# Optimization experiments

Measured on AMD Instinct MI355X. Metric: run time of the kernel, lower is better.

## Reference

```python
import jax, jax.numpy as jnp
import numpy as np
from jax import lax

NF = 64; LAT = 512; IMG = 64; NC = 4
DILS = (1, 2, 4, 8)                 # dilated 3x3 sobel: effective kernels 3,5,9,17 w/ pads 1,2,4,8
CF = 1 + 2 * len(DILS)              # identity + (sobel_x, sobel_y) per scale -> 9
FIN = NF * CF; FH = NF; FO = NF     # DynaResidualBlock dims
NFREQ = 6; FCH = 4 * NFREQ          # sin/cos over x and y per frequency -> 24 pos channels
CAT = LAT + NF * FCH                # input dim of out_to_lat blocks (512 + 1536 = 2048)
P_DYN = FH * FIN + FH + FO * FH + FO + FO * FIN + FO


def _make_pe():
    c = (np.arange(IMG, dtype=np.float32) + 0.5) / IMG
    yy, xx = np.meshgrid(c, c, indexing='ij')
    ch = []
    for u in (xx, yy):
        for f in range(NFREQ):
            w = (2.0 ** f) * 2.0 * np.pi
            ch.append(np.sin(w * u)); ch.append(np.cos(w * u))
    return jnp.asarray(np.stack(ch, 0).astype(np.float32))   # [FCH, H, W]


def _lin_res(x, w1, b1, w2, b2, ws, bs):
    # LinearResidualBlock: skip linear + 2-layer MLP with LeakyReLU(0.2)
    return x @ ws + bs + jax.nn.leaky_relu(x @ w1 + b1, 0.2) @ w2 + b2

_SX = jnp.array([[-1., 0., 1.], [-2., 0., 2.], [-1., 0., 1.]], jnp.float32) / 8.0
_SY = _SX.T


def _perceive(x):
    # multi-scale sobel perception (RandGrads): identity + depthwise dilated sobel x/y
    feats = [x]
    dn = ('NCHW', 'OIHW', 'NCHW')
    for d in DILS:
        for k in (_SX, _SY):
            kern = jnp.broadcast_to(k, (NF, 1, 3, 3))
            feats.append(lax.conv_general_dilated(
                x, kern, (1, 1), [(d, d), (d, d)],
                rhs_dilation=(d, d), dimension_numbers=dn,
                feature_group_count=NF))
    return jnp.concatenate(feats, axis=1)   # [B, NF*CF, H, W]


def _inorm(x, eps=1e-5):
    # InstanceNorm2d (affine=False)
    m = x.mean((2, 3), keepdims=True)
    v = ((x - m) ** 2).mean((2, 3), keepdims=True)
    return (x - m) * lax.rsqrt(v + eps)


def _dyna_conv(x, lat, dyn_w, dyn_b):
    # DynaResidualBlock: hypernetwork generates per-sample 1x1 conv weights from lat
    B = x.shape[0]
    p = lat @ dyn_w + dyn_b                 # [B, P_DYN]
    o = 0
    def take(n):
        nonlocal o
        q = p[:, o:o + n]; o += n; return q
    k_in = take(FH * FIN).reshape(B, FH, FIN); b_in = take(FH)
    k_out = take(FO * FH).reshape(B, FO, FH); b_out = take(FO)
    k_sk = take(FO * FIN).reshape(B, FO, FIN); b_sk = take(FO)
    h = jnp.einsum('bfi,bihw->bfhw', k_in, x) + b_in[:, :, None, None]
    h = jax.nn.leaky_relu(h, 0.2)
    y = jnp.einsum('bof,bfhw->bohw', k_out, h) + b_out[:, :, None, None]
    s = jnp.einsum('boi,bihw->bohw', k_sk, x) + b_sk[:, :, None, None]
    return s + y


def setup_inputs() -> dict:
    key = jax.random.key(0)
    ks = jax.random.split(key, 16)
    g = lambda i, shape, s=0.02: jax.random.normal(ks[i], shape, jnp.float32) * s
    z = lambda shape: jnp.zeros(shape, jnp.float32)
    return {
        'x': jax.random.normal(ks[0], (16, 3, IMG, IMG), jnp.float32),
        'inj_lat': jax.random.normal(ks[1], (16, LAT), jnp.float32),
        'w_in': g(2, (NF, 3), 0.3), 'b_in': z((NF,)),
        'fl_w1': g(3, (LAT, LAT)), 'fl_b1': z((LAT,)),
        'fl_w2': g(4, (LAT, LAT)), 'fl_b2': z((LAT,)),
        'fl_ws': g(5, (LAT, LAT)), 'fl_bs': z((LAT,)),
        'dyn_w': g(6, (LAT, P_DYN), 0.002), 'dyn_b': g(7, (P_DYN,), 0.002),
        'pe': _make_pe(),
        'otl_w1': g(8, (NC, CAT, CAT)), 'otl_b1': z((NC, CAT)),
        'otl_w2': g(9, (NC, CAT, LAT)), 'otl_b2': z((NC, LAT)),
        'otl_ws': g(10, (NC, CAT, LAT)), 'otl_bs': z((NC, LAT)),
        'ltl_w': g(11, (LAT, LAT)), 'ltl_b': z((LAT,)),
    }


def reference(x, inj_lat, w_in, b_in, fl_w1, fl_b1, fl_w2, fl_b2, fl_ws, fl_bs,
              dyn_w, dyn_b, pe, otl_w1, otl_b1, otl_w2, otl_b2, otl_ws, otl_bs,
              ltl_w, ltl_b):
    B = x.shape[0]
    out = jnp.einsum('oc,bchw->bohw', w_in, x) + b_in[None, :, None, None]  # in_conv (1x1)
    lat = jnp.zeros((B, LAT), x.dtype)
    for c in range(NC):
        inj_lat = _lin_res(inj_lat, fl_w1, fl_b1, fl_w2, fl_b2, fl_ws, fl_bs)
        out = _dyna_conv(_inorm(_perceive(out)), inj_lat, dyn_w, dyn_b)
        # ConvFreqEncoding(out).mean((2,3)) == contraction of out with pos encodings
        freq = jnp.einsum('bchw,fhw->bcf', out, pe).reshape(B, -1) / (IMG * IMG)
        lat = _lin_res(jnp.concatenate([lat, freq], axis=1),
                       otl_w1[c], otl_b1[c], otl_w2[c], otl_b2[c], otl_ws[c], otl_bs[c])
    return lat @ ltl_w + ltl_b
```

## Files before the change

### kernel.cpp

```cpp
#include <hip/hip_runtime.h>
#include <hip/hip_bf16.h>
#include <cstdint>
#include <cstddef>

#define PIX   4096
#define PDYN  78016
#define LATD  512
#define CATD  2048

typedef unsigned short u16;
typedef __attribute__((ext_vector_type(8))) short bf16x8;
typedef __attribute__((ext_vector_type(4))) float f32x4;
#define MFMA16(a,b,c) __builtin_amdgcn_mfma_f32_16x16x32_bf16(a,b,c,0,0,0)

__device__ __forceinline__ float lrelu(float v) { return v > 0.f ? v : 0.2f * v; }
__device__ __forceinline__ unsigned bfbits(float x) {
  __hip_bfloat16 h = __float2bfloat16(x);
  return (unsigned)*(unsigned short*)&h;
}
__device__ __forceinline__ unsigned pack2(float a, float b) {
  return bfbits(a) | (bfbits(b) << 16);
}

__global__ void k_zero(float* __restrict__ p, int n) {
  int i = blockIdx.x * 256 + threadIdx.x;
  if (i < n) p[i] = 0.f;
}

__global__ void k_init_out(const float* __restrict__ x, const float* __restrict__ w_in,
                           const float* __restrict__ b_in, float* __restrict__ out) {
  int idx = blockIdx.x * 256 + threadIdx.x;
  int p = idx & 4095, o = (idx >> 12) & 63, b = idx >> 18;
  const float* xb = x + (size_t)b * 3 * PIX + p;
  out[idx] = b_in[o] + w_in[o*3+0]*xb[0] + w_in[o*3+1]*xb[PIX] + w_in[o*3+2]*xb[2*PIX];
}

__global__ void k_cat_init(const float* __restrict__ lat, float* __restrict__ cat) {
  int idx = blockIdx.x * 256 + threadIdx.x;
  int j = idx & 2047, b = idx >> 11;
  cat[idx] = (j < 512) ? lat[b*512 + j] : 0.f;
}

__global__ void k_pe(const float* __restrict__ pe, u16* __restrict__ peB) {
  int idx = blockIdx.x * 256 + threadIdx.x;
  int j = idx & 7, lane = (idx >> 3) & 63, kc = (idx >> 9) & 3, ft = (idx >> 11) & 1, pt = idx >> 12;
  int f = ft*16 + (lane & 15);
  int p = pt*128 + kc*32 + (lane >> 4)*8 + j;
  peB[idx] = (f < 24) ? (u16)bfbits(pe[(size_t)f*PIX + p]) : (u16)0;
}

__global__ void k_afold(const float* __restrict__ inj_seq, u16* __restrict__ Abf) {
  int idx = blockIdx.x * 256 + threadIdx.x;
  int j = idx & 7, lane = (idx >> 3) & 63, mt = (idx >> 9) & 3, kc = (idx >> 11) & 1, kb = idx >> 12;
  int m = mt*16 + (lane & 15);
  int k = kb*64 + kc*32 + (lane >> 4)*8 + j;
  Abf[idx] = (u16)bfbits(inj_seq[m*512 + k]);
}

__device__ __forceinline__ void feat9(const float (*ch)[65], int h, int w, float* f) {
  f[0] = ch[h][w];
#pragma unroll
  for (int di = 0; di < 4; ++di) {
    int d = 1 << di;
    bool hm = (h - d) >= 0, hp = (h + d) < 64;
    bool wm = (w - d) >= 0, wp = (w + d) < 64;
    float tm = (hm && wm) ? ch[h-d][w-d] : 0.f;
    float t0 =  hm        ? ch[h-d][w  ] : 0.f;
    float tp = (hm && wp) ? ch[h-d][w+d] : 0.f;
    float mm =  wm        ? ch[h  ][w-d] : 0.f;
    float mp =  wp        ? ch[h  ][w+d] : 0.f;
    float bm = (hp && wm) ? ch[h+d][w-d] : 0.f;
    float b0 =  hp        ? ch[h+d][w  ] : 0.f;
    float bp = (hp && wp) ? ch[h+d][w+d] : 0.f;
    f[1 + 2*di] = (tp - tm + 2.f*(mp - mm) + bp - bm) * 0.125f;
    f[2 + 2*di] = (bm - tm + 2.f*(b0 - t0) + bp - tp) * 0.125f;
  }
}

__global__ __launch_bounds__(256) void k_prep(const float* __restrict__ out,
                                              __hip_bfloat16* __restrict__ xn) {
  __shared__ float ch[64][65];
  __shared__ float redS[4][9], redQ[4][9];
  __shared__ float mS[9], rS[9];
  int c = blockIdx.x, b = blockIdx.y, t = threadIdx.x;
  const float* src = out + ((size_t)b * 64 + c) * PIX;
  for (int j = 0; j < 16; ++j) { int idx = t + j*256; ch[idx >> 6][idx & 63] = src[idx]; }
  __syncthreads();
  float s[9], q[9];
#pragma unroll
  for (int k = 0; k < 9; ++k) { s[k] = 0.f; q[k] = 0.f; }
  for (int j = 0; j < 16; ++j) {
    int p = t + j*256; int h = p >> 6, w = p & 63;
    float f[9]; feat9(ch, h, w, f);
#pragma unroll
    for (int k = 0; k < 9; ++k) { s[k] += f[k]; q[k] += f[k]*f[k]; }
  }
#pragma unroll
  for (int off = 32; off; off >>= 1)
#pragma unroll
    for (int k = 0; k < 9; ++k) { s[k] += __shfl_down(s[k], off, 64); q[k] += __shfl_down(q[k], off, 64); }
  int lane = t & 63, wv = t >> 6;
  if (lane == 0)
#pragma unroll
    for (int k = 0; k < 9; ++k) { redS[wv][k] = s[k]; redQ[wv][k] = q[k]; }
  __syncthreads();
  if (t < 9) {
    float ss = 0.f, qq = 0.f;
    for (int w2 = 0; w2 < 4; ++w2) { ss += redS[w2][t]; qq += redQ[w2][t]; }
    float mean = ss * (1.f/4096.f);
    float var  = qq * (1.f/4096.f) - mean*mean;
    mS[t] = mean; rS[t] = rsqrtf(var + 1e-5f);
  }
  __syncthreads();
  for (int j = 0; j < 16; ++j) {
    int p = t + j*256; int h = p >> 6, w = p & 63;
    float f[9]; feat9(ch, h, w, f);
#pragma unroll
    for (int k = 0; k < 9; ++k)
      xn[((size_t)b * 576 + k*64 + c) * PIX + p] = __float2bfloat16((f[k] - mS[k]) * rS[k]);
  }
}

__global__ __launch_bounds__(256) void k_pgemm(
    const u16* __restrict__ Abf, const float* __restrict__ Bw,
    const float* __restrict__ bias, u16* __restrict__ Wst4,
    u16* __restrict__ KoutF4, float* __restrict__ biasf4) {
  __shared__ u16 Xl[128 * 64];
  int t = threadIdx.x;
  int lane = t & 63, wv = t >> 6;
  int col = lane & 15, quad = lane >> 4;
  int n0 = blockIdx.x * 128;
  int pg = t & 15, kq = t >> 4;

  f32x4 acc[4][2];
#pragma unroll
  for (int i = 0; i < 4; ++i) { acc[i][0] = {0.f,0.f,0.f,0.f}; acc[i][1] = {0.f,0.f,0.f,0.f}; }

  bool vld = (n0 + pg*8) < PDYN;

  for (int kb = 0; kb < 8; ++kb) {
    float br[4][8];
#pragma unroll
    for (int kk = 0; kk < 4; ++kk) {
      const float* src = Bw + (size_t)(kb*64 + kq*4 + kk)*PDYN + n0 + pg*8;
      float4 a0 = vld ? *(const float4*)src       : float4{0.f,0.f,0.f,0.f};
      float4 a1 = vld ? *(const float4*)(src + 4) : float4{0.f,0.f,0.f,0.f};
      br[kk][0]=a0.x; br[kk][1]=a0.y; br[kk][2]=a0.z; br[kk][3]=a0.w;
      br[kk][4]=a1.x; br[kk][5]=a1.y; br[kk][6]=a1.z; br[kk][7]=a1.w;
    }
    __syncthreads();
    int ch0 = kq >> 1, sub = (kq & 1) * 4;
#pragma unroll
    for (int jj = 0; jj < 8; ++jj) {
      int i = (jj + pg) & 7;
      unsigned lo = pack2(br[0][i], br[1][i]);
      unsigned hi = pack2(br[2][i], br[3][i]);
      int p = pg*8 + i;
      *(uint2*)&Xl[p*64 + ((ch0 ^ i) * 8) + sub] = make_uint2(lo, hi);
    }
    __syncthreads();
#pragma unroll
    for (int kc = 0; kc < 2; ++kc) {
      bf16x8 bfr[2];
#pragma unroll
      for (int nt = 0; nt < 2; ++nt) {
        int n = wv*32 + nt*16 + col;
        bfr[nt] = *(const bf16x8*)&Xl[n*64 + (((kc*4 + quad) ^ (n & 7)) * 8)];
      }
#pragma unroll
      for (int mt = 0; mt < 4; ++mt) {
        bf16x8 af = *(const bf16x8*)&Abf[(((kb*2 + kc)*4 + mt)*64 + lane) * 8];
        acc[mt][0] = MFMA16(af, bfr[0], acc[mt][0]);
        acc[mt][1] = MFMA16(af, bfr[1], acc[mt][1]);
      }
    }
  }

#pragma unroll
  for (int nt = 0; nt < 2; ++nt) {
    int pcol = n0 + wv*32 + nt*16 + col;
    if (pcol >= PDYN) continue;
    float bb = bias[pcol];
#pragma unroll
    for (int mt = 0; mt < 4; ++mt) {
#pragma unroll
      for (int r = 0; r < 4; ++r) {
        int lb = mt*16 + quad*4 + r;
        float v = acc[mt][nt][r] + bb;
        if (pcol < 36864) {
          int o = pcol / 576, f = pcol - o*576;
          Wst4[(size_t)lb*73728 + (f>>5)*4096 + o*32 + (f&31)] = (u16)bfbits(v);
        } else if (pcol < 36928) {
          biasf4[lb*192 + (pcol - 36864)] = v;
        } else if (pcol < 41024) {
          int q = pcol - 36928; int o = q >> 6, m = q & 63;
          int lk = ((m & 31) >> 3)*16 + (o & 15);
          KoutF4[(size_t)lb*4096 + (((o>>4)*2 + (m>>5))*64 + lk)*8 + (m & 7)] = (u16)bfbits(v);
        } else if (pcol < 41088) {
          biasf4[lb*192 + 64 + (pcol - 41024)] = v;
        } else if (pcol < 77952) {
          int q = pcol - 41088; int o = q / 576, f = q - o*576;
          Wst4[(size_t)lb*73728 + (f>>5)*4096 + (64 + o)*32 + (f&31)] = (u16)bfbits(v);
        } else {
          biasf4[lb*192 + 128 + (pcol - 77952)] = v;
        }
      }
    }
  }
}

__global__ __launch_bounds__(256) void k_dyna(
    const u16* __restrict__ Wst4, const u16* __restrict__ xn,
    const u16* __restrict__ KoutF4, const u16* __restrict__ peB,
    const float* __restrict__ biasf4, float* __restrict__ out,
    float* __restrict__ cat, int cyc) {
  __shared__ u16 lds[16384];
  u16* As = lds;
  u16* Xl = lds + 8192;

  int t = threadIdx.x;
  int lane = t & 63, wv = t >> 6;
  int col = lane & 15, quad = lane >> 4;
  int b = blockIdx.y, p0 = blockIdx.x * 128;

  const u16* WB  = Wst4 + (size_t)(cyc*16 + b) * 73728;
  const u16* xnB = xn  + (size_t)b * 576 * PIX + p0;

  f32x4 acc[8][2];
#pragma unroll
  for (int i = 0; i < 8; ++i) { acc[i][0] = {0.f,0.f,0.f,0.f}; acc[i][1] = {0.f,0.f,0.f,0.f}; }

  int sm = t & 127, skg = t >> 7, s7 = sm & 7;
  int pg = t & 15, kq = t >> 4;
  (void)skg; (void)sm; (void)s7;

  for (int kb = 0; kb < 9; ++kb) {
    uint4 w[4];
    const uint4* wsrc = (const uint4*)(WB + (size_t)kb*8192 + t*32);
#pragma unroll
    for (int q = 0; q < 4; ++q) w[q] = wsrc[q];
    uint4 xr[4];
#pragma unroll
    for (int kk = 0; kk < 4; ++kk)
      xr[kk] = *(const uint4*)(xnB + (size_t)(kb*64 + kq*4 + kk)*PIX + pg*8);
    __syncthreads();
    {
      int m = t & 127, kg = t >> 7, m7 = m & 7;
#pragma unroll
      for (int q = 0; q < 4; ++q)
        *(uint4*)&As[m*64 + (((kg*4 + q) ^ m7) * 8)] = w[q];
    }
    const unsigned* xw = (const unsigned*)xr;
    unsigned pkl[8], pkh[8];
#pragma unroll
    for (int i = 0; i < 8; ++i) {
      unsigned sh = (i & 1) * 16;
      unsigned h0 = (xw[0  + (i>>1)] >> sh) & 0xffffu;
      unsigned h1 = (xw[4  + (i>>1)] >> sh) & 0xffffu;
      unsigned h2 = (xw[8  + (i>>1)] >> sh) & 0xffffu;
      unsigned h3 = (xw[12 + (i>>1)] >> sh) & 0xffffu;
      pkl[i] = h0 | (h1 << 16);
      pkh[i] = h2 | (h3 << 16);
    }
    int ch0 = kq >> 1, sub = (kq & 1) * 4;
#pragma unroll
    for (int jj = 0; jj < 8; ++jj) {
      int i = (jj + pg) & 7;
      int p = pg*8 + i;
      *(uint2*)&Xl[p*64 + ((ch0 ^ i) * 8) + sub] = make_uint2(pkl[i], pkh[i]);
    }
    __syncthreads();
#pragma unroll
    for (int kc = 0; kc < 2; ++kc) {
      bf16x8 bfr[2];
#pragma unroll
      for (int nt = 0; nt < 2; ++nt) {
        int n = wv*32 + nt*16 + col;
        bfr[nt] = *(const bf16x8*)&Xl[n*64 + (((kc*4 + quad) ^ (n & 7)) * 8)];
      }
#pragma unroll
      for (int mt = 0; mt < 8; ++mt) {
        int m = mt*16 + col;
        bf16x8 af = *(const bf16x8*)&As[m*64 + (((kc*4 + quad) ^ (m & 7)) * 8)];
        acc[mt][0] = MFMA16(af, bfr[0], acc[mt][0]);
        acc[mt][1] = MFMA16(af, bfr[1], acc[mt][1]);
      }
    }
  }
  __syncthreads();

  const float* bfB = biasf4 + (size_t)(cyc*16 + b) * 192;
#pragma unroll
  for (int mt = 0; mt < 4; ++mt) {
    float bm[4];
#pragma unroll
    for (int r = 0; r < 4; ++r) bm[r] = bfB[mt*16 + quad*4 + r];
#pragma unroll
    for (int nt = 0; nt < 2; ++nt) {
      unsigned lo = pack2(lrelu(acc[mt][nt][0] + bm[0]), lrelu(acc[mt][nt][1] + bm[1]));
      unsigned hi = pack2(lrelu(acc[mt][nt][2] + bm[2]), lrelu(acc[mt][nt][3] + bm[3]));
      int nl = nt*16 + col;
      int ch = (mt*2 + (quad >> 1)) ^ (nl & 7);
      *(uint2*)&As[(wv*32 + nl)*64 + ch*8 + (quad & 1)*4] = make_uint2(lo, hi);
    }
  }
  __syncthreads();

  f32x4 yac[4][2];
#pragma unroll
  for (int i = 0; i < 4; ++i) { yac[i][0] = {0.f,0.f,0.f,0.f}; yac[i][1] = {0.f,0.f,0.f,0.f}; }
  const u16* kofB = KoutF4 + (size_t)(cyc*16 + b) * 4096;
#pragma unroll
  for (int kc = 0; kc < 2; ++kc) {
    bf16x8 hb[2];
#pragma unroll
    for (int nt = 0; nt < 2; ++nt) {
      int nl = nt*16 + col;
      hb[nt] = *(const bf16x8*)&As[(wv*32 + nl)*64 + (((kc*4 + quad) ^ (nl & 7)) * 8)];
    }
#pragma unroll
    for (int ot = 0; ot < 4; ++ot) {
      bf16x8 ka = *(const bf16x8*)&kofB[((ot*2 + kc)*64 + lane) * 8];
      yac[ot][0] = MFMA16(ka, hb[0], yac[ot][0]);
      yac[ot][1] = MFMA16(ka, hb[1], yac[ot][1]);
    }
  }
#pragma unroll
  for (int ot = 0; ot < 4; ++ot) {
    float bo[4];
#pragma unroll
    for (int r = 0; r < 4; ++r) {
      int o = ot*16 + quad*4 + r;
      bo[r] = bfB[64 + o] + bfB[128 + o];
    }
#pragma unroll
    for (int nt = 0; nt < 2; ++nt) {
      int pl = wv*32 + nt*16 + col;
#pragma unroll
      for (int r = 0; r < 4; ++r) {
        float rs = acc[4 + ot][nt][r] + yac[ot][nt][r] + bo[r];
        int o = ot*16 + quad*4 + r;
        out[((size_t)b*64 + o)*PIX + p0 + pl] = rs;
        Xl[o*128 + (((pl >> 3) ^ (o & 7)) * 8) + (pl & 7)] = (u16)bfbits(rs);
      }
    }
  }
  __syncthreads();

  f32x4 fac[4][2];
#pragma unroll
  for (int i = 0; i < 4; ++i) { fac[i][0] = {0.f,0.f,0.f,0.f}; fac[i][1] = {0.f,0.f,0.f,0.f}; }
  bf16x8 pb[2];
#pragma unroll
  for (int ft = 0; ft < 2; ++ft)
    pb[ft] = *(const bf16x8*)&peB[((((size_t)blockIdx.x*2 + ft)*4 + wv)*64 + lane) * 8];
#pragma unroll
  for (int mt = 0; mt < 4; ++mt) {
    int o = mt*16 + col;
    bf16x8 ar = *(const bf16x8*)&Xl[o*128 + (((wv*4 + quad) ^ (o & 7)) * 8)];
    fac[mt][0] = MFMA16(ar, pb[0], fac[mt][0]);
    fac[mt][1] = MFMA16(ar, pb[1], fac[mt][1]);
  }
  __syncthreads();
  float* fred = (float*)lds;
#pragma unroll
  for (int mt = 0; mt < 4; ++mt)
#pragma unroll
    for (int ft = 0; ft < 2; ++ft)
#pragma unroll
      for (int r = 0; r < 4; ++r)
        fred[(wv*64 + mt*16 + quad*4 + r)*32 + ft*16 + col] = fac[mt][ft][r];
  __syncthreads();
  for (int pr = t; pr < 1536; pr += 256) {
    int o = pr / 24, f = pr - o*24;
    float s = fred[o*32 + f] + fred[(64 + o)*32 + f] + fred[(128 + o)*32 + f] + fred[(192 + o)*32 + f];
    atomicAdd(&cat[b*CATD + 512 + o*24 + f], s * (1.f/4096.f));
  }
}

__global__ __launch_bounds__(256) void gemm_skinny(
    const float* __restrict__ A, const float* __restrict__ Bm,
    float* __restrict__ C, int N, int K) {
  __shared__ float As[16][17];
  __shared__ float Bs[16][64];
  int t = threadIdx.x;
  int row = t & 15, cg = t >> 4;
  int n0 = blockIdx.x * 64;
  int ks = gridDim.y;
  int kchunk = K / ks;
  int k0base = blockIdx.y * kchunk;
  float acc[4] = {0.f, 0.f, 0.f, 0.f};
  for (int k0 = k0base; k0 < k0base + kchunk; k0 += 16) {
    { int lr = t >> 4, lc = t & 15; As[lc][lr] = A[(size_t)lr*K + k0 + lc]; }
#pragma unroll
    for (int j = 0; j < 4; ++j) {
      int idx = t + j*256;
      int kr = idx >> 6, nc = idx & 63;
      Bs[kr][nc] = Bm[(size_t)(k0 + kr)*N + n0 + nc];
    }
    __syncthreads();
#pragma unroll
    for (int kk = 0; kk < 16; ++kk) {
      float a = As[kk][row];
      float4 bv = *(const float4*)&Bs[kk][cg*4];
      acc[0] += a*bv.x; acc[1] += a*bv.y; acc[2] += a*bv.z; acc[3] += a*bv.w;
    }
    __syncthreads();
  }
  float* Pp = C + (size_t)blockIdx.y * 16 * N;
#pragma unroll
  for (int j = 0; j < 4; ++j) Pp[(size_t)row*N + n0 + cg*4 + j] = acc[j];
}

__global__ __launch_bounds__(256) void gemm_skinny2(
    const float* __restrict__ A,
    const float* __restrict__ B1, float* __restrict__ C1, int N1, int tiles1,
    const float* __restrict__ B2, float* __restrict__ C2, int N2, int K) {
  __shared__ float As[16][17];
  __shared__ float Bs[16][64];
  int bx = blockIdx.x;
  const float* Bm; float* C; int N, n0;
  if (bx < tiles1) { Bm = B1; C = C1; N = N1; n0 = bx*64; }
  else             { Bm = B2; C = C2; N = N2; n0 = (bx - tiles1)*64; }
  int t = threadIdx.x;
  int row = t & 15, cg = t >> 4;
  int ks = gridDim.y;
  int kchunk = K / ks;
  int k0base = blockIdx.y * kchunk;
  float acc[4] = {0.f, 0.f, 0.f, 0.f};
  for (int k0 = k0base; k0 < k0base + kchunk; k0 += 16) {
    { int lr = t >> 4, lc = t & 15; As[lc][lr] = A[(size_t)lr*K + k0 + lc]; }
#pragma unroll
    for (int j = 0; j < 4; ++j) {
      int idx = t + j*256;
      int kr = idx >> 6, nc = idx & 63;
      Bs[kr][nc] = Bm[(size_t)(k0 + kr)*N + n0 + nc];
    }
    __syncthreads();
#pragma unroll
    for (int kk = 0; kk < 16; ++kk) {
      float a = As[kk][row];
      float4 bv = *(const float4*)&Bs[kk][cg*4];
      acc[0] += a*bv.x; acc[1] += a*bv.y; acc[2] += a*bv.z; acc[3] += a*bv.w;
    }
    __syncthreads();
  }
  float* Pp = C + (size_t)blockIdx.y * 16 * N;
#pragma unroll
  for (int j = 0; j < 4; ++j) Pp[(size_t)row*N + n0 + cg*4 + j] = acc[j];
}

__global__ void k_reduce(float* __restrict__ C,
                         const float* __restrict__ P1, int ns1, const float* __restrict__ bias1,
                         const float* __restrict__ P2, int ns2, const float* __restrict__ bias2,
                         int nmask, int total, int act, int accum) {
  int idx = blockIdx.x * 256 + threadIdx.x;
  if (idx >= total) return;
  int col = idx & nmask;
  float v = bias1[col];
  for (int s = 0; s < ns1; ++s) v += P1[(size_t)s*total + idx];
  if (P2) { v += bias2[col]; for (int s = 0; s < ns2; ++s) v += P2[(size_t)s*total + idx]; }
  if (act) v = lrelu(v);
  if (accum) v += C[idx];
  C[idx] = v;
}

extern "C" void kernel_launch(void* const* d_in, const int* in_sizes, int n_in,
                              void* d_out, int out_size, void* d_ws, size_t ws_size,
                              hipStream_t stream) {
  const float* x      = (const float*)d_in[0];
  const float* inj0   = (const float*)d_in[1];
  const float* w_in   = (const float*)d_in[2];
  const float* b_in   = (const float*)d_in[3];
  const float* fl_w1  = (const float*)d_in[4];
  const float* fl_b1  = (const float*)d_in[5];
  const float* fl_w2  = (const float*)d_in[6];
  const float* fl_b2  = (const float*)d_in[7];
  const float* fl_ws  = (const float*)d_in[8];
  const float* fl_bs  = (const float*)d_in[9];
  const float* dyn_w  = (const float*)d_in[10];
  const float* dyn_b  = (const float*)d_in[11];
  const float* pe     = (const float*)d_in[12];
  const float* otl_w1 = (const float*)d_in[13];
  const float* otl_b1 = (const float*)d_in[14];
  const float* otl_w2 = (const float*)d_in[15];
  const float* otl_b2 = (const float*)d_in[16];
  const float* otl_ws = (const float*)d_in[17];
  const float* otl_bs = (const float*)d_in[18];
  const float* ltl_w  = (const float*)d_in[19];
  const float* ltl_b  = (const float*)d_in[20];
  float* outF = (float*)d_out;

  char* w = (char*)d_ws;
  float* inj_seq = (float*)(w + 0);
  float* tmpA    = (float*)(w + 131072);
  float* lat     = (float*)(w + 262144);
  float* cat     = (float*)(w + 294912);
  float* biasf4  = (float*)(w + 425984);
  float* part1   = (float*)(w + 475136);
  float* part2   = (float*)(w + 2572288);
  float* part3   = (float*)(w + 3096576);
  u16*   Wst4    = (u16*)  (w + 3620864);
  u16*   KoutF4  = (u16*)  (w + 13058048);
  u16*   Abf     = (u16*)  (w + 13582336);
  u16*   peB     = (u16*)  (w + 13647872);
  float* outb    = (float*)(w + 13910016);
  u16*   xnb     = (u16*)  (w + 30687232);

  k_zero<<<32, 256, 0, stream>>>(lat, 16*512);
  k_init_out<<<16384, 256, 0, stream>>>(x, w_in, b_in, outb);
  k_pe<<<512, 256, 0, stream>>>(pe, peB);

  for (int c = 0; c < 4; ++c) {
    const float* src = (c == 0) ? inj0 : (inj_seq + (size_t)(c-1)*16*LATD);
    float* dst = inj_seq + (size_t)c*16*LATD;
    gemm_skinny2<<<dim3(16,8), 256, 0, stream>>>(src, fl_w1, part2, 512, 8, fl_ws, part3, 512, 512);
    k_reduce<<<32, 256, 0, stream>>>(tmpA, part2, 8, fl_b1, nullptr, 0, nullptr, 511, 8192, 1, 0);
    gemm_skinny<<<dim3(8,8), 256, 0, stream>>>(tmpA, fl_w2, part2, 512, 512);
    k_reduce<<<32, 256, 0, stream>>>(dst, part3, 8, fl_bs, part2, 8, fl_b2, 511, 8192, 0, 0);
  }
  k_afold<<<128, 256, 0, stream>>>(inj_seq, Abf);
  k_pgemm<<<610, 256, 0, stream>>>(Abf, dyn_w, dyn_b, Wst4, KoutF4, biasf4);

  for (int c = 0; c < 4; ++c) {
    k_prep<<<dim3(64,16), 256, 0, stream>>>(outb, (__hip_bfloat16*)xnb);
    k_cat_init<<<128, 256, 0, stream>>>(lat, cat);
    k_dyna<<<dim3(32,16), 256, 0, stream>>>(Wst4, xnb, KoutF4, peB, biasf4, outb, cat, c);
    gemm_skinny2<<<dim3(40,16), 256, 0, stream>>>(cat, otl_w1 + (size_t)c*CATD*CATD, part1, 2048, 32,
                                                  otl_ws + (size_t)c*CATD*LATD, part3, 512, 2048);
    k_reduce<<<128, 256, 0, stream>>>(tmpA, part1, 16, otl_b1 + c*CATD,
                                      nullptr, 0, nullptr, 2047, 16*2048, 1, 0);
    gemm_skinny<<<dim3(8,16), 256, 0, stream>>>(tmpA, otl_w2 + (size_t)c*CATD*LATD, part2, 512, 2048);
    k_reduce<<<32, 256, 0, stream>>>(lat, part3, 16, otl_bs + c*LATD,
                                     part2, 16, otl_b2 + c*LATD, 511, 16*512, 0, 0);
  }
  gemm_skinny<<<dim3(8,8), 256, 0, stream>>>(lat, ltl_w, part2, 512, 512);
  k_reduce<<<32, 256, 0, stream>>>(outF, part2, 8, ltl_b, nullptr, 0, nullptr, 511, 8192, 0, 0);
}
```

Measured before the change: 916.8 us.

## Load hypernet B operand directly into MFMA registers and add MFMA skinny GEMM

k_pgemm no longer stages the fp32 dyn_w tile through LDS with two barriers per k-block. Each lane now loads its 8 strided K values per column straight from global memory and packs them to bf16 in registers for the MFMA. A new k_mgemm16 kernel computes the 2048x2048 otl_w1 product for the 16-row batch with bf16 MFMA and an 8-way K split, replacing the fused gemm_skinny2; the otl_ws product moves to a separate gemm_skinny launch. The goal is to cut LDS traffic and sync overhead on these weight-bandwidth-bound GEMMs. The cost is per-lane strided global loads with less vectorisation per instruction, bf16 rounding of the cat activations, and one extra launch per cycle.

```diff
diff --git a/kernel.cpp b/kernel.cpp
--- a/kernel.cpp
+++ b/kernel.cpp
@@ -21,6 +21,7 @@
 __device__ __forceinline__ unsigned pack2(float a, float b) {
   return bfbits(a) | (bfbits(b) << 16);
 }
+union bfcast { unsigned u[4]; bf16x8 v; };
 
 __global__ void k_zero(float* __restrict__ p, int n) {
   int i = blockIdx.x * 256 + threadIdx.x;
@@ -125,60 +126,54 @@
     const u16* __restrict__ Abf, const float* __restrict__ Bw,
     const float* __restrict__ bias, u16* __restrict__ Wst4,
     u16* __restrict__ KoutF4, float* __restrict__ biasf4) {
-  __shared__ u16 Xl[128 * 64];
   int t = threadIdx.x;
   int lane = t & 63, wv = t >> 6;
   int col = lane & 15, quad = lane >> 4;
   int n0 = blockIdx.x * 128;
-  int pg = t & 15, kq = t >> 4;
 
   f32x4 acc[4][2];
 #pragma unroll
   for (int i = 0; i < 4; ++i) { acc[i][0] = {0.f,0.f,0.f,0.f}; acc[i][1] = {0.f,0.f,0.f,0.f}; }
 
-  bool vld = (n0 + pg*8) < PDYN;
+  int nn[2]; bool vld[2]; size_t loff[2];
+#pragma unroll
+  for (int nt = 0; nt < 2; ++nt) {
+    nn[nt] = n0 + wv*32 + nt*16 + col;
+    vld[nt] = nn[nt] < PDYN;
+    loff[nt] = (size_t)(quad*8)*PDYN + nn[nt];
+  }
 
   for (int kb = 0; kb < 8; ++kb) {
-    float br[4][8];
-#pragma unroll
-    for (int kk = 0; kk < 4; ++kk) {
-      const float* src = Bw + (size_t)(kb*64 + kq*4 + kk)*PDYN + n0 + pg*8;
-      float4 a0 = vld ? *(const float4*)src       : float4{0.f,0.f,0.f,0.f};
-      float4 a1 = vld ? *(const float4*)(src + 4) : float4{0.f,0.f,0.f,0.f};
-      br[kk][0]=a0.x; br[kk][1]=a0.y; br[kk][2]=a0.z; br[kk][3]=a0.w;
-      br[kk][4]=a1.x; br[kk][5]=a1.y; br[kk][6]=a1.z; br[kk][7]=a1.w;
-    }
-    __syncthreads();
-    int ch0 = kq >> 1, sub = (kq & 1) * 4;
-#pragma unroll
-    for (int jj = 0; jj < 8; ++jj) {
-      int i = (jj + pg) & 7;
-      unsigned lo = pack2(br[0][i], br[1][i]);
-      unsigned hi = pack2(br[2][i], br[3][i]);
-      int p = pg*8 + i;
-      *(uint2*)&Xl[p*64 + ((ch0 ^ i) * 8) + sub] = make_uint2(lo, hi);
-    }
-    __syncthreads();
+    float bv[2][2][8];
 #pragma unroll
     for (int kc = 0; kc < 2; ++kc) {
-      bf16x8 bfr[2];
-#pragma unroll
-      for (int nt = 0; nt < 2; ++nt) {
-        int n = wv*32 + nt*16 + col;
-        bfr[nt] = *(const bf16x8*)&Xl[n*64 + (((kc*4 + quad) ^ (n & 7)) * 8)];
-      }
+      const float* Brow = Bw + (size_t)(kb*64 + kc*32)*PDYN;
+#pragma unroll
+      for (int nt = 0; nt < 2; ++nt)
+#pragma unroll
+        for (int j = 0; j < 8; ++j)
+          bv[kc][nt][j] = vld[nt] ? Brow[(size_t)j*PDYN + loff[nt]] : 0.f;
+    }
+#pragma unroll
+    for (int kc = 0; kc < 2; ++kc) {
+      bfcast bfr[2];
+#pragma unroll
+      for (int nt = 0; nt < 2; ++nt)
+#pragma unroll
+        for (int u = 0; u < 4; ++u)
+          bfr[nt].u[u] = pack2(bv[kc][nt][2*u], bv[kc][nt][2*u+1]);
 #pragma unroll
       for (int mt = 0; mt < 4; ++mt) {
         bf16x8 af = *(const bf16x8*)&Abf[(((kb*2 + kc)*4 + mt)*64 + lane) * 8];
-        acc[mt][0] = MFMA16(af, bfr[0], acc[mt][0]);
-        acc[mt][1] = MFMA16(af, bfr[1], acc[mt][1]);
+        acc[mt][0] = MFMA16(af, bfr[0].v, acc[mt][0]);
+        acc[mt][1] = MFMA16(af, bfr[1].v, acc[mt][1]);
       }
     }
   }
 
 #pragma unroll
   for (int nt = 0; nt < 2; ++nt) {
-    int pcol = n0 + wv*32 + nt*16 + col;
+    int pcol = nn[nt];
     if (pcol >= PDYN) continue;
     float bb = bias[pcol];
 #pragma unroll
@@ -209,6 +204,50 @@
   }
 }
 
+__global__ __launch_bounds__(256) void k_mgemm16(
+    const float* __restrict__ A, const float* __restrict__ Bw,
+    float* __restrict__ Cp, int N, int K) {
+  int t = threadIdx.x;
+  int lane = t & 63, wv = t >> 6;
+  int col = lane & 15, quad = lane >> 4;
+  int n0 = blockIdx.x * 128;
+  int kchunk = K / gridDim.y;
+  int kbeg = blockIdx.y * kchunk;
+
+  f32x4 acc[2] = {{0.f,0.f,0.f,0.f},{0.f,0.f,0.f,0.f}};
+  int n = n0 + wv*32 + col;
+  size_t loff = (size_t)(quad*8)*N + n;
+  const float* Arow = A + col*K + quad*8;
+
+  for (int k0 = kbeg; k0 < kbeg + kchunk; k0 += 64) {
+#pragma unroll
+    for (int kc = 0; kc < 2; ++kc) {
+      float4 a0 = *(const float4*)(Arow + k0 + kc*32);
+      float4 a1 = *(const float4*)(Arow + k0 + kc*32 + 4);
+      bfcast af;
+      af.u[0] = pack2(a0.x, a0.y); af.u[1] = pack2(a0.z, a0.w);
+      af.u[2] = pack2(a1.x, a1.y); af.u[3] = pack2(a1.z, a1.w);
+      const float* Brow = Bw + (size_t)(k0 + kc*32)*N;
+#pragma unroll
+      for (int nt = 0; nt < 2; ++nt) {
+        float bj[8];
+#pragma unroll
+        for (int j = 0; j < 8; ++j) bj[j] = Brow[(size_t)j*N + loff + nt*16];
+        bfcast bfr;
+#pragma unroll
+        for (int u = 0; u < 4; ++u) bfr.u[u] = pack2(bj[2*u], bj[2*u+1]);
+        acc[nt] = MFMA16(af.v, bfr.v, acc[nt]);
+      }
+    }
+  }
+  float* Cb = Cp + (size_t)blockIdx.y * 16 * N;
+#pragma unroll
+  for (int nt = 0; nt < 2; ++nt)
+#pragma unroll
+    for (int r = 0; r < 4; ++r)
+      Cb[(size_t)(quad*4 + r)*N + n + nt*16] = acc[nt][r];
+}
+
 __global__ __launch_bounds__(256) void k_dyna(
     const u16* __restrict__ Wst4, const u16* __restrict__ xn,
     const u16* __restrict__ KoutF4, const u16* __restrict__ peB,
@@ -230,9 +269,7 @@
 #pragma unroll
   for (int i = 0; i < 8; ++i) { acc[i][0] = {0.f,0.f,0.f,0.f}; acc[i][1] = {0.f,0.f,0.f,0.f}; }
 
-  int sm = t & 127, skg = t >> 7, s7 = sm & 7;
   int pg = t & 15, kq = t >> 4;
-  (void)skg; (void)sm; (void)s7;
 
   for (int kb = 0; kb < 9; ++kb) {
     uint4 w[4];
@@ -526,9 +563,9 @@
     k_prep<<<dim3(64,16), 256, 0, stream>>>(outb, (__hip_bfloat16*)xnb);
     k_cat_init<<<128, 256, 0, stream>>>(lat, cat);
     k_dyna<<<dim3(32,16), 256, 0, stream>>>(Wst4, xnb, KoutF4, peB, biasf4, outb, cat, c);
-    gemm_skinny2<<<dim3(40,16), 256, 0, stream>>>(cat, otl_w1 + (size_t)c*CATD*CATD, part1, 2048, 32,
-                                                  otl_ws + (size_t)c*CATD*LATD, part3, 512, 2048);
-    k_reduce<<<128, 256, 0, stream>>>(tmpA, part1, 16, otl_b1 + c*CATD,
+    k_mgemm16<<<dim3(16,8), 256, 0, stream>>>(cat, otl_w1 + (size_t)c*CATD*CATD, part1, 2048, 2048);
+    gemm_skinny<<<dim3(8,16), 256, 0, stream>>>(cat, otl_ws + (size_t)c*CATD*LATD, part3, 512, 2048);
+    k_reduce<<<128, 256, 0, stream>>>(tmpA, part1, 8, otl_b1 + c*CATD,
                                       nullptr, 0, nullptr, 2047, 16*2048, 1, 0);
     gemm_skinny<<<dim3(8,16), 256, 0, stream>>>(tmpA, otl_w2 + (size_t)c*CATD*LATD, part2, 512, 2048);
     k_reduce<<<32, 256, 0, stream>>>(lat, part3, 16, otl_bs + c*LATD,
```

Result: slower. 1.010 ms (+10.2%).
